# Performance work log

Hardware: AMD Instinct MI355X
Metric: run time of the kernel (lower is better)

## Reference

```python
import jax, jax.numpy as jnp
import numpy as np

GAMMA = 0.997
N_STEPS = 5
EPS = 1e-3
Q_WEIGHTS = np.array([1.0, 0.5, 0.0, 2.0], dtype=np.float32)


def _rescale(x):
    # sign(x) * (sqrt(|x|+1) - 1) + eps * x
    return jnp.sign(x) * (jnp.sqrt(jnp.abs(x) + 1.0) - 1.0) + EPS * x


def _inv_rescale(x):
    sign = jnp.sign(x)
    sqrt_arg = 1.0 + 4.0 * EPS * (jnp.abs(x) + 1.0 + EPS)
    square = ((jnp.sqrt(sqrt_arg) - 1.0) / (2.0 * EPS)) ** 2
    return sign * (square - 1.0)


def setup_inputs() -> dict:
    key = jax.random.key(0)
    ks = jax.random.split(key, 6)
    B, T, Q = 4096, 512, 4
    current_q_value = jax.random.normal(ks[0], (B, T, Q), dtype=jnp.float32)
    next_q_value = jax.random.normal(ks[1], (B, T, Q), dtype=jnp.float32)
    log_p = jax.random.normal(ks[2], (B, T), dtype=jnp.float32)
    reward = jax.random.normal(ks[3], (B, T, Q), dtype=jnp.float32)
    is_done = jax.random.bernoulli(ks[4], 0.02, (B, T)).astype(jnp.float32)
    mask = jax.random.bernoulli(ks[5], 0.95, (B, T)).astype(jnp.float32)
    return {
        "current_q_value": current_q_value,
        "next_q_value": next_q_value,
        "log_p": log_p,
        "reward": reward,
        "is_done": is_done,
        "mask": mask,
    }


def reference(current_q_value, next_q_value, log_p, reward, is_done, mask):
    B, T, Q = reward.shape
    q_w = jnp.asarray(Q_WEIGHTS)[None, None, :]                     # (1,1,Q)
    nz = (q_w != 0)
    inv_qw = jnp.where(nz, 1.0 / jnp.where(nz, q_w, 1.0), 0.0)      # (1,1,Q)
    inv_num_q = 1.0 / float((Q_WEIGHTS != 0).sum())

    m = mask[..., None]                                             # (B,T,1)
    d = is_done[..., None]                                          # (B,T,1)

    nq = m * (1.0 - d) * _inv_rescale(next_q_value)                 # (B,T,Q)
    lp = inv_num_q * inv_qw * (m * (1.0 - d) * log_p[..., None])    # (B,T,Q)

    pad = jnp.zeros((B, N_STEPS - 1, Q), dtype=reward.dtype)
    pad_reward = jnp.concatenate([m * reward, pad], axis=1)         # (B,T+n-1,Q)
    lp_pad = jnp.concatenate([lp, pad], axis=1)                     # (B,T+n-1,Q)

    gpow = GAMMA ** jnp.arange(N_STEPS, dtype=jnp.float32)          # gamma^0..gamma^{n-1}
    widx = jnp.arange(T)[:, None] + jnp.arange(N_STEPS)[None, :]    # (T,n) window indices

    reward_sum = jnp.einsum('btnq,n->btq', pad_reward[:, widx, :], gpow)
    log_p_sum = jnp.einsum('btnq,n->btq', lp_pad[:, widx, :], gpow * GAMMA)

    idxs = jnp.minimum(T - 1, jnp.arange(T) + N_STEPS - 1)          # (T,)
    # NOTE: original code uses gamma**idx (absolute index), reproduced faithfully
    next_term = (GAMMA ** idxs.astype(jnp.float32))[None, :, None] * nq[:, idxs, :]

    target = _rescale(reward_sum + next_term + log_p_sum)           # (B,T,Q)
    loss = 0.5 * m * q_w * (current_q_value - target) ** 2
    return loss
```

## Files before the change

kernel.cpp:

```cpp
#include <hip/hip_runtime.h>
#include <math.h>

#define T_DIM 512
#define T_SHIFT 9
#define GAMMA_F 0.997f
#define EPS_F 1e-3f
#define LOG2_GAMMA (-0.0043345903f)

__device__ __forceinline__ float inv_rescale_f(float x) {
    float s = (x > 0.f) ? 1.f : ((x < 0.f) ? -1.f : 0.f);
    float sqrt_arg = 1.f + 4.f * EPS_F * (fabsf(x) + 1.f + EPS_F);
    float q = (sqrtf(sqrt_arg) - 1.f) * (1.f / (2.f * EPS_F));
    return s * (q * q - 1.f);
}

__device__ __forceinline__ float rescale_f(float x) {
    return copysignf(sqrtf(fabsf(x) + 1.f) - 1.f, x) + EPS_F * x;
}

__global__ __launch_bounds__(256) void nstep_qloss_kernel(
    const float* __restrict__ cur_q,
    const float* __restrict__ next_q,
    const float* __restrict__ log_p,
    const float* __restrict__ reward,
    const float* __restrict__ is_done,
    const float* __restrict__ mask,
    float* __restrict__ out,
    int BT)
{
    int idx = blockIdx.x * 256 + threadIdx.x;
    if (idx >= BT) return;
    int t = idx & (T_DIM - 1);
    int base = idx - t;

    const float g1 = GAMMA_F;
    const float g2 = g1 * g1;
    const float g3 = g2 * g1;
    const float g4 = g2 * g2;
    const float gpow[5] = {1.f, g1, g2, g3, g4};

    const float4* reward4 = (const float4*)reward;
    const float4* curq4   = (const float4*)cur_q;
    const float4* nextq4  = (const float4*)next_q;
    float4* out4          = (float4*)out;

    float rs0 = 0.f, rs1 = 0.f, rs2 = 0.f, rs3 = 0.f;
    float Lsum = 0.f;
    float m_t = 0.f;

#pragma unroll
    for (int j = 0; j < 5; ++j) {
        int s = t + j;
        if (s < T_DIM) {
            int o = base + s;
            float mm = mask[o];
            float dd = is_done[o];
            float lp = log_p[o];
            float4 r = reward4[o];
            if (j == 0) m_t = mm;
            float w = gpow[j] * mm;
            rs0 += w * r.x;
            rs1 += w * r.y;
            rs2 += w * r.z;
            rs3 += w * r.w;
            Lsum += (gpow[j] * GAMMA_F) * (mm * (1.f - dd) * lp);
        }
    }

    int i = t + 4; if (i > T_DIM - 1) i = T_DIM - 1;
    int oi = base + i;
    float mi = mask[oi];
    float di = is_done[oi];
    float coeff = exp2f((float)i * LOG2_GAMMA);
    float g = coeff * mi * (1.f - di);
    float4 nq = nextq4[oi];
    float nt0 = g * inv_rescale_f(nq.x);
    float nt1 = g * inv_rescale_f(nq.y);
    float nt2 = g * inv_rescale_f(nq.z);
    float nt3 = g * inv_rescale_f(nq.w);

    const float inv_num_q = 1.f / 3.f;
    float Ls = inv_num_q * Lsum;
    float tgt0 = rescale_f(rs0 + nt0 + 1.0f * Ls);
    float tgt1 = rescale_f(rs1 + nt1 + 2.0f * Ls);
    float tgt2 = rescale_f(rs2 + nt2 + 0.0f * Ls);
    float tgt3 = rescale_f(rs3 + nt3 + 0.5f * Ls);

    float4 cq = curq4[idx];
    float4 o;
    float hm = 0.5f * m_t;
    float d0 = cq.x - tgt0;
    float d1 = cq.y - tgt1;
    float d2 = cq.z - tgt2;  (void)d2;
    float d3 = cq.w - tgt3;
    o.x = hm * 1.0f * d0 * d0;
    o.y = hm * 0.5f * d1 * d1;
    o.z = 0.f;
    o.w = hm * 2.0f * d3 * d3;
    out4[idx] = o;
}

extern "C" void kernel_launch(void* const* d_in, const int* in_sizes, int n_in,
                              void* d_out, int out_size, void* d_ws, size_t ws_size,
                              hipStream_t stream) {
    const float* cur_q   = (const float*)d_in[0];
    const float* next_q  = (const float*)d_in[1];
    const float* log_p   = (const float*)d_in[2];
    const float* reward  = (const float*)d_in[3];
    const float* is_done = (const float*)d_in[4];
    const float* mask    = (const float*)d_in[5];
    float* out = (float*)d_out;

    int BT = in_sizes[2];
    int blocks = (BT + 255) / 256;
    hipLaunchKernelGGL(nstep_qloss_kernel, dim3(blocks), dim3(256), 0, stream,
                       cur_q, next_q, log_p, reward, is_done, mask, out, BT);
}
```

Measured before the change: 168.0 us.

## Process four timesteps per thread and reuse the reward window in registers

Each thread now computes four consecutive timesteps instead of one. It loads mask, done and log_p as float4 vectors, and loads an 8-entry reward window once so the overlapping 5-step windows share it instead of reloading. The end-of-row boundary is handled by zeroing the high mask and clamping the next-Q index. Outputs use nontemporal stores. The aim is to cut redundant global loads and scalar load instructions, at the cost of higher register use, 4x fewer threads, and per-thread strided (less coalesced) access.

```diff
diff --git a/kernel.cpp b/kernel.cpp
--- a/kernel.cpp
+++ b/kernel.cpp
@@ -2,10 +2,11 @@
 #include <math.h>
 
 #define T_DIM 512
-#define T_SHIFT 9
 #define GAMMA_F 0.997f
 #define EPS_F 1e-3f
-#define LOG2_GAMMA (-0.0043345903f)
+#define LOG2_GAMMA (-0.0043345907f)
+
+typedef float v4f __attribute__((ext_vector_type(4)));
 
 __device__ __forceinline__ float inv_rescale_f(float x) {
     float s = (x > 0.f) ? 1.f : ((x < 0.f) ? -1.f : 0.f);
@@ -26,78 +27,116 @@
     const float* __restrict__ is_done,
     const float* __restrict__ mask,
     float* __restrict__ out,
-    int BT)
+    int nthreads)
 {
-    int idx = blockIdx.x * 256 + threadIdx.x;
-    if (idx >= BT) return;
-    int t = idx & (T_DIM - 1);
-    int base = idx - t;
+    int tid = blockIdx.x * 256 + threadIdx.x;
+    if (tid >= nthreads) return;
+
+    int tg = tid & (T_DIM / 4 - 1);
+    int t0 = tg << 2;
+    int rowBase = (tid >> 7) << 9;
+
+    const v4f* mask4 = (const v4f*)mask;
+    const v4f* done4 = (const v4f*)is_done;
+    const v4f* lp4   = (const v4f*)log_p;
+    const v4f* rew4  = (const v4f*)reward;
+    const v4f* nq4   = (const v4f*)next_q;
+    const v4f* cq4   = (const v4f*)cur_q;
+    v4f* out4        = (v4f*)out;
+
+    const bool atEnd = (t0 == T_DIM - 4);
+
+    int v0 = tid;
+    int v1 = atEnd ? v0 : (v0 + 1);
+    v4f mlo = mask4[v0], mhi = mask4[v1];
+    v4f dlo = done4[v0], dhi = done4[v1];
+    v4f plo = lp4[v0],   phi = lp4[v1];
+    if (atEnd) { mhi = (v4f)(0.f); }
+
+    int eb = rowBase + t0;
+    v4f r[8];
+    r[0] = rew4[eb + 0]; r[1] = rew4[eb + 1]; r[2] = rew4[eb + 2]; r[3] = rew4[eb + 3];
+    {
+        int hb = atEnd ? (rowBase + T_DIM - 1) : (eb + 4);
+        int hs = atEnd ? 0 : 1;
+        r[4] = rew4[hb];
+        r[5] = rew4[hb + hs];
+        r[6] = rew4[hb + 2 * hs];
+        r[7] = rew4[hb + 3 * hs];
+    }
+
+    float mv[8]  = { mlo.x, mlo.y, mlo.z, mlo.w, mhi.x, mhi.y, mhi.z, mhi.w };
+    float Lm[8];
+    Lm[0] = mlo.x * (1.f - dlo.x) * plo.x;
+    Lm[1] = mlo.y * (1.f - dlo.y) * plo.y;
+    Lm[2] = mlo.z * (1.f - dlo.z) * plo.z;
+    Lm[3] = mlo.w * (1.f - dlo.w) * plo.w;
+    Lm[4] = mhi.x * (1.f - dhi.x) * phi.x;
+    Lm[5] = mhi.y * (1.f - dhi.y) * phi.y;
+    Lm[6] = mhi.z * (1.f - dhi.z) * phi.z;
+    Lm[7] = mhi.w * (1.f - dhi.w) * phi.w;
 
     const float g1 = GAMMA_F;
     const float g2 = g1 * g1;
     const float g3 = g2 * g1;
     const float g4 = g2 * g2;
-    const float gpow[5] = {1.f, g1, g2, g3, g4};
+    const float gpow[5] = { 1.f, g1, g2, g3, g4 };
 
-    const float4* reward4 = (const float4*)reward;
-    const float4* curq4   = (const float4*)cur_q;
-    const float4* nextq4  = (const float4*)next_q;
-    float4* out4          = (float4*)out;
+    float mhiA[4] = { mhi.x, mhi.y, mhi.z, mhi.w };
+    float dhiA[4] = { dhi.x, dhi.y, dhi.z, dhi.w };
 
-    float rs0 = 0.f, rs1 = 0.f, rs2 = 0.f, rs3 = 0.f;
-    float Lsum = 0.f;
-    float m_t = 0.f;
+    v4f cq[4];
+    cq[0] = cq4[eb + 0]; cq[1] = cq4[eb + 1]; cq[2] = cq4[eb + 2]; cq[3] = cq4[eb + 3];
+    v4f nq[4];
+    int iClamp = rowBase + T_DIM - 1;
+#pragma unroll
+    for (int j = 0; j < 4; ++j) {
+        int ii = atEnd ? iClamp : (eb + 4 + j);
+        nq[j] = nq4[ii];
+    }
+
+    const float inv_num_q = 1.f / 3.f;
 
 #pragma unroll
-    for (int j = 0; j < 5; ++j) {
-        int s = t + j;
-        if (s < T_DIM) {
-            int o = base + s;
-            float mm = mask[o];
-            float dd = is_done[o];
-            float lp = log_p[o];
-            float4 r = reward4[o];
-            if (j == 0) m_t = mm;
-            float w = gpow[j] * mm;
-            rs0 += w * r.x;
-            rs1 += w * r.y;
-            rs2 += w * r.z;
-            rs3 += w * r.w;
-            Lsum += (gpow[j] * GAMMA_F) * (mm * (1.f - dd) * lp);
+    for (int j = 0; j < 4; ++j) {
+        float a0 = 0.f, a1 = 0.f, a2 = 0.f, a3 = 0.f, Ls = 0.f;
+#pragma unroll
+        for (int k = 0; k < 5; ++k) {
+            float w = gpow[k] * mv[j + k];
+            a0 = fmaf(w, r[j + k].x, a0);
+            a1 = fmaf(w, r[j + k].y, a1);
+            a2 = fmaf(w, r[j + k].z, a2);
+            a3 = fmaf(w, r[j + k].w, a3);
+            Ls = fmaf(gpow[k], Lm[j + k], Ls);
         }
+        Ls *= GAMMA_F * inv_num_q;
+
+        int i = atEnd ? (T_DIM - 1) : (t0 + 4 + j);
+        float moi = atEnd ? mlo.w : mhiA[j];
+        float doi = atEnd ? dlo.w : dhiA[j];
+        float coeff = exp2f((float)i * LOG2_GAMMA);
+        float g = coeff * moi * (1.f - doi);
+        float nt0 = g * inv_rescale_f(nq[j].x);
+        float nt1 = g * inv_rescale_f(nq[j].y);
+        float nt2 = g * inv_rescale_f(nq[j].z);
+        float nt3 = g * inv_rescale_f(nq[j].w);
+
+        float tgt0 = rescale_f(a0 + nt0 + 1.0f * Ls);
+        float tgt1 = rescale_f(a1 + nt1 + 2.0f * Ls);
+        float tgt2 = rescale_f(a2 + nt2);
+        float tgt3 = rescale_f(a3 + nt3 + 0.5f * Ls);
+
+        float hm = 0.5f * mv[j];
+        float d0 = cq[j].x - tgt0;
+        float d1 = cq[j].y - tgt1;
+        float d3 = cq[j].w - tgt3;
+        v4f o;
+        o.x = hm * d0 * d0;
+        o.y = hm * 0.5f * d1 * d1;
+        o.z = 0.f;
+        o.w = hm * 2.0f * d3 * d3;
+        __builtin_nontemporal_store(o, &out4[eb + j]);
     }
-
-    int i = t + 4; if (i > T_DIM - 1) i = T_DIM - 1;
-    int oi = base + i;
-    float mi = mask[oi];
-    float di = is_done[oi];
-    float coeff = exp2f((float)i * LOG2_GAMMA);
-    float g = coeff * mi * (1.f - di);
-    float4 nq = nextq4[oi];
-    float nt0 = g * inv_rescale_f(nq.x);
-    float nt1 = g * inv_rescale_f(nq.y);
-    float nt2 = g * inv_rescale_f(nq.z);
-    float nt3 = g * inv_rescale_f(nq.w);
-
-    const float inv_num_q = 1.f / 3.f;
-    float Ls = inv_num_q * Lsum;
-    float tgt0 = rescale_f(rs0 + nt0 + 1.0f * Ls);
-    float tgt1 = rescale_f(rs1 + nt1 + 2.0f * Ls);
-    float tgt2 = rescale_f(rs2 + nt2 + 0.0f * Ls);
-    float tgt3 = rescale_f(rs3 + nt3 + 0.5f * Ls);
-
-    float4 cq = curq4[idx];
-    float4 o;
-    float hm = 0.5f * m_t;
-    float d0 = cq.x - tgt0;
-    float d1 = cq.y - tgt1;
-    float d2 = cq.z - tgt2;  (void)d2;
-    float d3 = cq.w - tgt3;
-    o.x = hm * 1.0f * d0 * d0;
-    o.y = hm * 0.5f * d1 * d1;
-    o.z = 0.f;
-    o.w = hm * 2.0f * d3 * d3;
-    out4[idx] = o;
 }
 
 extern "C" void kernel_launch(void* const* d_in, const int* in_sizes, int n_in,
@@ -112,7 +151,8 @@
     float* out = (float*)d_out;
 
     int BT = in_sizes[2];
-    int blocks = (BT + 255) / 256;
+    int nthreads = BT / 4;
+    int blocks = (nthreads + 255) / 256;
     hipLaunchKernelGGL(nstep_qloss_kernel, dim3(blocks), dim3(256), 0, stream,
-                       cur_q, next_q, log_p, reward, is_done, mask, out, BT);
+                       cur_q, next_q, log_p, reward, is_done, mask, out, nthreads);
 }
```

After: 207.6 us. 23.6% more time.
